# Optimization experiments

Hardware: AMD Instinct MI355X
Metric: run time of the kernel (lower is better)

The kernel has to match this reference:

```python
import jax, jax.numpy as jnp
import numpy as np

N_NODES = 100000
N_EDGES = 1600000
N_GRAPHS = 256
F_IN = 128
HID = 128


def gcn_conv(x, W, b, src, dst, n_nodes):
    """PyG GCNConv: h = D^{-1/2}(A+I)D^{-1/2} (x @ W) + b, self-loops added."""
    h = x @ W  # [N, H]
    ones = jnp.ones((src.shape[0],), dtype=x.dtype)
    deg = jax.ops.segment_sum(ones, dst, num_segments=n_nodes) + 1.0  # +1 self-loop
    dinv = jax.lax.rsqrt(deg)  # deg >= 1 always
    norm = dinv[src] * dinv[dst]  # [E]
    msgs = h[src] * norm[:, None]  # gather + scale, [E, H]
    agg = jax.ops.segment_sum(msgs, dst, num_segments=n_nodes)  # scatter-add
    agg = agg + h * (dinv * dinv)[:, None]  # self-loop contribution
    return agg + b


def setup_inputs() -> dict:
    key = jax.random.key(0)
    ks = jax.random.split(key, 8)
    x = jax.random.normal(ks[0], (N_NODES, F_IN), dtype=jnp.float32)
    edge_index = jax.random.randint(ks[1], (2, N_EDGES), 0, N_NODES, dtype=jnp.int64)
    batch = jnp.sort(jax.random.randint(ks[2], (N_NODES,), 0, N_GRAPHS, dtype=jnp.int64))
    s1 = 1.0 / np.sqrt(F_IN)
    s2 = 1.0 / np.sqrt(HID)
    w1 = jax.random.normal(ks[3], (F_IN, HID), dtype=jnp.float32) * s1
    b1 = jnp.zeros((HID,), dtype=jnp.float32)
    w2 = jax.random.normal(ks[4], (HID, HID), dtype=jnp.float32) * s2
    b2 = jnp.zeros((HID,), dtype=jnp.float32)
    w_out = jax.random.normal(ks[5], (HID, 1), dtype=jnp.float32) * s2
    b_out = jnp.zeros((1,), dtype=jnp.float32)
    return {"x": x, "edge_index": edge_index, "batch": batch,
            "w1": w1, "b1": b1, "w2": w2, "b2": b2,
            "w_out": w_out, "b_out": b_out}


def reference(x, edge_index, batch, w1, b1, w2, b2, w_out, b_out):
    src, dst = edge_index[0], edge_index[1]
    n = x.shape[0]
    h = jax.nn.relu(gcn_conv(x, w1, b1, src, dst, n))
    h = jax.nn.relu(gcn_conv(h, w2, b2, src, dst, n))
    # global mean pool over graphs
    sums = jax.ops.segment_sum(h, batch, num_segments=N_GRAPHS)  # [G, H]
    counts = jax.ops.segment_sum(jnp.ones((n,), dtype=h.dtype), batch, num_segments=N_GRAPHS)
    pooled = sums / jnp.maximum(counts, 1.0)[:, None]
    return pooled @ w_out + b_out  # [G, 1]
```

## Files before the change

### kernel.cpp

```cpp
#include <hip/hip_runtime.h>
#include <hip/hip_fp16.h>

#define N_NODES 100000
#define N_EDGES 1600000
#define N_GRAPHS 256
#define NB 1563
#define SBLOCKS 256
#define GB1 782

typedef _Float16 half8 __attribute__((ext_vector_type(8)));
typedef float f32x4 __attribute__((ext_vector_type(4)));

__device__ __forceinline__ unsigned pack2(float a, float b) {
    __half2 h = __floats2half2_rn(a, b);
    return *reinterpret_cast<unsigned*>(&h);
}

__global__ __launch_bounds__(256) void wprep_kernel(const float* __restrict__ W1,
                                                    const float* __restrict__ W2,
                                                    __half* __restrict__ Wt1,
                                                    __half* __restrict__ Wt2) {
    int b = blockIdx.x;
    const float* W = (b < 64) ? W1 : W2;
    __half* Wt = (b < 64) ? Wt1 : Wt2;
    int t = (b & 63) * 256 + threadIdx.x;
    int n = t >> 7, k = t & 127;
    Wt[t] = (__half)W[k * 128 + n];
}

__global__ __launch_bounds__(256) void gemmhist_kernel(const float* __restrict__ Xf,
                                                       const __half* __restrict__ Xh,
                                                       const __half* __restrict__ Wt,
                                                       const float* __restrict__ dinv,
                                                       __half* __restrict__ HT,
                                                       int xf16, int withDinv,
                                                       const int* __restrict__ dst,
                                                       int* __restrict__ cnt2d,
                                                       int histBlocks) {
    __shared__ __align__(16) char smem[69632];
    const int tid = threadIdx.x;
    int bid = blockIdx.x;
    bool isHist = false;
    int id = bid;
    if (histBlocks) {
        if (bid < 1024) {
            if ((bid & 3) == 0) { isHist = true; id = bid >> 2; }
            else id = (bid >> 2) * 3 + (bid & 3) - 1;
        } else {
            id = 768 + (bid - 1024);
        }
    }

    if (isHist) {
        int* lcnt = (int*)smem;
        for (int i = tid; i < NB; i += 256) lcnt[i] = 0;
        __syncthreads();
        const int per = (N_EDGES + SBLOCKS - 1) / SBLOCKS;
        int e0 = id * per, e1 = min(e0 + per, N_EDGES);
        for (int e = e0 + tid; e < e1; e += 256)
            atomicAdd(&lcnt[dst[e] >> 6], 1);
        __syncthreads();
        for (int i = tid; i < NB; i += 256)
            cnt2d[id * NB + i] = lcnt[i];
        return;
    }

    typedef __half (*TileT)[136];
    TileT Xl = (TileT)smem;
    TileT Wl = (TileT)(smem + 34816);
    const int row0 = id * 128;

#pragma unroll
    for (int i = 0; i < 8; ++i) {
        int idx = tid + i * 256;
        int n = idx >> 4, c0 = (idx & 15) * 8;
        *(uint4*)&Wl[n][c0] = *(const uint4*)&Wt[n * 128 + c0];
    }
    if (xf16) {
#pragma unroll
        for (int i = 0; i < 8; ++i) {
            int idx = tid + i * 256;
            int r = idx >> 4, c0 = (idx & 15) * 8;
            int rr = min(row0 + r, N_NODES - 1);
            *(uint4*)&Xl[r][c0] = *(const uint4*)&Xh[(size_t)rr * 128 + c0];
        }
    } else {
#pragma unroll
        for (int i = 0; i < 16; ++i) {
            int idx = tid + i * 256;
            int r = idx >> 5, c0 = (idx & 31) * 4;
            int rr = min(row0 + r, N_NODES - 1);
            float4 v = *(const float4*)&Xf[(size_t)rr * 128 + c0];
            uint2 o;
            o.x = pack2(v.x, v.y);
            o.y = pack2(v.z, v.w);
            *(uint2*)&Xl[r][c0] = o;
        }
    }
    __syncthreads();

    const int wv = tid >> 6;
    const int lane = tid & 63;
    const int lr = lane & 15;
    const int lg = lane >> 4;

    f32x4 acc[2][8];
#pragma unroll
    for (int mt = 0; mt < 2; ++mt)
#pragma unroll
        for (int nt = 0; nt < 8; ++nt) acc[mt][nt] = (f32x4){0.f, 0.f, 0.f, 0.f};

#pragma unroll
    for (int ks = 0; ks < 4; ++ks) {
        const int kb = ks * 32 + lg * 8;
        half8 a0 = *reinterpret_cast<const half8*>(&Xl[wv * 32 + lr][kb]);
        half8 a1 = *reinterpret_cast<const half8*>(&Xl[wv * 32 + 16 + lr][kb]);
        half8 b[8];
#pragma unroll
        for (int nt = 0; nt < 8; ++nt)
            b[nt] = *reinterpret_cast<const half8*>(&Wl[nt * 16 + lr][kb]);
#pragma unroll
        for (int nt = 0; nt < 8; ++nt) {
            acc[0][nt] = __builtin_amdgcn_mfma_f32_16x16x32_f16(a0, b[nt], acc[0][nt], 0, 0, 0);
            acc[1][nt] = __builtin_amdgcn_mfma_f32_16x16x32_f16(a1, b[nt], acc[1][nt], 0, 0, 0);
        }
    }

#pragma unroll
    for (int mt = 0; mt < 2; ++mt) {
#pragma unroll
        for (int i = 0; i < 4; ++i) {
            int rr = row0 + wv * 32 + mt * 16 + lg * 4 + i;
            if (rr < N_NODES) {
                float di = withDinv ? dinv[rr] : 1.0f;
#pragma unroll
                for (int nt = 0; nt < 8; ++nt)
                    HT[(size_t)rr * 128 + nt * 16 + lr] = (__half)(acc[mt][nt][i] * di);
            }
        }
    }
}

__global__ __launch_bounds__(256) void scan2d_kernel(int* __restrict__ cnt2d,
                                                     int* __restrict__ bucket_cnt) {
    __shared__ int ts[256];
    int i = blockIdx.x;
    int t = threadIdx.x;
    int v = cnt2d[t * NB + i];
    ts[t] = v;
    __syncthreads();
    for (int off = 1; off < 256; off <<= 1) {
        int y = (t >= off) ? ts[t - off] : 0;
        __syncthreads();
        ts[t] += y;
        __syncthreads();
    }
    cnt2d[t * NB + i] = ts[t] - v;
    if (t == 255) bucket_cnt[i] = ts[255];
}

#define BVPT 7
__global__ __launch_bounds__(256) void scatter_kernel(const int* __restrict__ src,
                                                      const int* __restrict__ dst,
                                                      const int* __restrict__ cnt2d,
                                                      const int* __restrict__ bucket_cnt,
                                                      int* __restrict__ bucket_off,
                                                      unsigned* __restrict__ pairbuf) {
    __shared__ int lcur[NB];
    __shared__ int tsum[256];
    const int tid = threadIdx.x;
    const int blk = blockIdx.x;

    int v[BVPT];
    int s = 0;
#pragma unroll
    for (int j = 0; j < BVPT; ++j) {
        int idx = tid * BVPT + j;
        v[j] = (idx < NB) ? bucket_cnt[idx] : 0;
        s += v[j];
    }
    tsum[tid] = s;
    __syncthreads();
    for (int off = 1; off < 256; off <<= 1) {
        int y = (tid >= off) ? tsum[tid - off] : 0;
        __syncthreads();
        tsum[tid] += y;
        __syncthreads();
    }
    int run = (tid > 0) ? tsum[tid - 1] : 0;
#pragma unroll
    for (int j = 0; j < BVPT; ++j) {
        int idx = tid * BVPT + j;
        if (idx < NB) {
            lcur[idx] = run + cnt2d[blk * NB + idx];
            if (blk == 0) bucket_off[idx] = run;
        }
        run += v[j];
    }
    if (blk == 0 && tid == 255) bucket_off[NB] = tsum[255];
    __syncthreads();

    const int per = (N_EDGES + SBLOCKS - 1) / SBLOCKS;
    int e0 = blk * per, e1 = min(e0 + per, N_EDGES);
    for (int e = e0 + tid; e < e1; e += 256) {
        int d = dst[e];
        int b = d >> 6;
        int p = atomicAdd(&lcur[b], 1);
        pairbuf[p] = ((unsigned)(d & 63) << 17) | (unsigned)src[e];
    }
}

__global__ __launch_bounds__(256) void localsort_kernel(const unsigned* __restrict__ pairbuf,
                                                        const int* __restrict__ bucket_off,
                                                        int* __restrict__ csr_src,
                                                        int* __restrict__ row_off,
                                                        float* __restrict__ dinv) {
    __shared__ int ldeg[64];
    __shared__ int lcur[64];
    int tid = threadIdx.x;
    int b = blockIdx.x;
    int base = bucket_off[b];
    int cnt = bucket_off[b + 1] - base;
    const unsigned* pb = pairbuf + base;
    int n0 = b << 6;

    if (tid < 64) ldeg[tid] = 0;
    __syncthreads();
    for (int i = tid; i < cnt; i += 256)
        atomicAdd(&ldeg[pb[i] >> 17], 1);
    __syncthreads();
    if (tid < 64) {
        int d = ldeg[tid];
        int x = d;
#pragma unroll
        for (int off = 1; off < 64; off <<= 1) {
            int y = __shfl_up(x, off);
            if (tid >= off) x += y;
        }
        int ex = x - d;
        lcur[tid] = ex;
        int n = n0 + tid;
        if (n < N_NODES) {
            row_off[n] = base + ex;
            dinv[n] = rsqrtf((float)d + 1.0f);
        }
    }
    __syncthreads();
    for (int i = tid; i < cnt; i += 256) {
        unsigned w = pb[i];
        int dl = w >> 17;
        int s = (int)(w & 0x1FFFFu);
        int p = atomicAdd(&lcur[dl], 1);
        csr_src[base + p] = s;
    }
}

__device__ __forceinline__ void add8(float* a, uint4 w) {
    float2 p0 = __half22float2(*reinterpret_cast<__half2*>(&w.x));
    float2 p1 = __half22float2(*reinterpret_cast<__half2*>(&w.y));
    float2 p2 = __half22float2(*reinterpret_cast<__half2*>(&w.z));
    float2 p3 = __half22float2(*reinterpret_cast<__half2*>(&w.w));
    a[0] += p0.x; a[1] += p0.y; a[2] += p1.x; a[3] += p1.y;
    a[4] += p2.x; a[5] += p2.y; a[6] += p3.x; a[7] += p3.y;
}
__device__ __forceinline__ void fma8(float* a, uint4 w, float s) {
    float2 p0 = __half22float2(*reinterpret_cast<__half2*>(&w.x));
    float2 p1 = __half22float2(*reinterpret_cast<__half2*>(&w.y));
    float2 p2 = __half22float2(*reinterpret_cast<__half2*>(&w.z));
    float2 p3 = __half22float2(*reinterpret_cast<__half2*>(&w.w));
    a[0] = fmaf(s, p0.x, a[0]); a[1] = fmaf(s, p0.y, a[1]);
    a[2] = fmaf(s, p1.x, a[2]); a[3] = fmaf(s, p1.y, a[3]);
    a[4] = fmaf(s, p2.x, a[4]); a[5] = fmaf(s, p2.y, a[5]);
    a[6] = fmaf(s, p3.x, a[6]); a[7] = fmaf(s, p3.y, a[7]);
}

__global__ __launch_bounds__(256) void gather1_kernel(const int* __restrict__ row_off,
                                                      const int* __restrict__ csr_src,
                                                      const __half* __restrict__ ht,
                                                      const float* __restrict__ dinv,
                                                      const float* __restrict__ bias,
                                                      __half* __restrict__ Y) {
    int t = blockIdx.x * 256 + threadIdx.x;
    int n = t >> 4;
    if (n >= N_NODES) return;
    int f = (t & 15) * 8;
    int e0 = row_off[n];
    int e1 = (n < N_NODES - 1) ? row_off[n + 1] : N_EDGES;
    const __half* htf = ht + f;
    float dn = dinv[n];

    float a0[8] = {0,0,0,0,0,0,0,0};
    float a1[8] = {0,0,0,0,0,0,0,0};
    float a2[8] = {0,0,0,0,0,0,0,0};
    float a3[8] = {0,0,0,0,0,0,0,0};
    fma8(a0, *(const uint4*)&htf[(size_t)n * 128], dn);

    int e = e0;
    for (; e + 4 <= e1; e += 4) {
        int s0 = csr_src[e], s1 = csr_src[e + 1];
        int s2 = csr_src[e + 2], s3 = csr_src[e + 3];
        uint4 w0 = *(const uint4*)&htf[(size_t)s0 * 128];
        uint4 w1 = *(const uint4*)&htf[(size_t)s1 * 128];
        uint4 w2 = *(const uint4*)&htf[(size_t)s2 * 128];
        uint4 w3 = *(const uint4*)&htf[(size_t)s3 * 128];
        fma8(a0, w0, dinv[s0]); fma8(a1, w1, dinv[s1]);
        fma8(a2, w2, dinv[s2]); fma8(a3, w3, dinv[s3]);
    }
    for (; e < e1; ++e) {
        int s = csr_src[e];
        fma8(a0, *(const uint4*)&htf[(size_t)s * 128], dinv[s]);
    }

    float4 bb0 = *(const float4*)&bias[f];
    float4 bb1 = *(const float4*)&bias[f + 4];
    float r0 = fmaxf((a0[0]+a1[0]+a2[0]+a3[0]) * dn + bb0.x, 0.0f);
    float r1 = fmaxf((a0[1]+a1[1]+a2[1]+a3[1]) * dn + bb0.y, 0.0f);
    float r2 = fmaxf((a0[2]+a1[2]+a2[2]+a3[2]) * dn + bb0.z, 0.0f);
    float r3 = fmaxf((a0[3]+a1[3]+a2[3]+a3[3]) * dn + bb0.w, 0.0f);
    float r4 = fmaxf((a0[4]+a1[4]+a2[4]+a3[4]) * dn + bb1.x, 0.0f);
    float r5 = fmaxf((a0[5]+a1[5]+a2[5]+a3[5]) * dn + bb1.y, 0.0f);
    float r6 = fmaxf((a0[6]+a1[6]+a2[6]+a3[6]) * dn + bb1.z, 0.0f);
    float r7 = fmaxf((a0[7]+a1[7]+a2[7]+a3[7]) * dn + bb1.w, 0.0f);
    uint4 o;
    o.x = pack2(r0, r1);
    o.y = pack2(r2, r3);
    o.z = pack2(r4, r5);
    o.w = pack2(r6, r7);
    *(uint4*)&Y[(size_t)n * 128 + f] = o;
}

__global__ __launch_bounds__(256) void gather2_kernel(const int* __restrict__ row_off,
                                                      const int* __restrict__ csr_src,
                                                      const __half* __restrict__ ht,
                                                      const float* __restrict__ dinv,
                                                      const float* __restrict__ bias,
                                                      __half* __restrict__ Y) {
    int t = blockIdx.x * 256 + threadIdx.x;
    int n = t >> 4;
    if (n >= N_NODES) return;
    int f = (t & 15) * 8;
    int e0 = row_off[n];
    int e1 = (n < N_NODES - 1) ? row_off[n + 1] : N_EDGES;
    const __half* htf = ht + f;
    float dn = dinv[n];

    float a0[8] = {0,0,0,0,0,0,0,0};
    float a1[8] = {0,0,0,0,0,0,0,0};
    float a2[8] = {0,0,0,0,0,0,0,0};
    float a3[8] = {0,0,0,0,0,0,0,0};
    add8(a0, *(const uint4*)&htf[(size_t)n * 128]);

    int e = e0;
    for (; e + 4 <= e1; e += 4) {
        int s0 = csr_src[e], s1 = csr_src[e + 1];
        int s2 = csr_src[e + 2], s3 = csr_src[e + 3];
        uint4 w0 = *(const uint4*)&htf[(size_t)s0 * 128];
        uint4 w1 = *(const uint4*)&htf[(size_t)s1 * 128];
        uint4 w2 = *(const uint4*)&htf[(size_t)s2 * 128];
        uint4 w3 = *(const uint4*)&htf[(size_t)s3 * 128];
        add8(a0, w0); add8(a1, w1); add8(a2, w2); add8(a3, w3);
    }
    for (; e < e1; ++e)
        add8(a0, *(const uint4*)&htf[(size_t)csr_src[e] * 128]);

    float4 bb0 = *(const float4*)&bias[f];
    float4 bb1 = *(const float4*)&bias[f + 4];
    float r0 = fmaxf((a0[0]+a1[0]+a2[0]+a3[0]) * dn + bb0.x, 0.0f);
    float r1 = fmaxf((a0[1]+a1[1]+a2[1]+a3[1]) * dn + bb0.y, 0.0f);
    float r2 = fmaxf((a0[2]+a1[2]+a2[2]+a3[2]) * dn + bb0.z, 0.0f);
    float r3 = fmaxf((a0[3]+a1[3]+a2[3]+a3[3]) * dn + bb0.w, 0.0f);
    float r4 = fmaxf((a0[4]+a1[4]+a2[4]+a3[4]) * dn + bb1.x, 0.0f);
    float r5 = fmaxf((a0[5]+a1[5]+a2[5]+a3[5]) * dn + bb1.y, 0.0f);
    float r6 = fmaxf((a0[6]+a1[6]+a2[6]+a3[6]) * dn + bb1.z, 0.0f);
    float r7 = fmaxf((a0[7]+a1[7]+a2[7]+a3[7]) * dn + bb1.w, 0.0f);
    uint4 o;
    o.x = pack2(r0, r1);
    o.y = pack2(r2, r3);
    o.z = pack2(r4, r5);
    o.w = pack2(r6, r7);
    *(uint4*)&Y[(size_t)n * 128 + f] = o;
}

__global__ __launch_bounds__(256) void poolout_kernel(const __half* __restrict__ Y,
                                                      const int* __restrict__ batch,
                                                      const float* __restrict__ w_out,
                                                      const float* __restrict__ b_out,
                                                      float* __restrict__ out) {
    __shared__ float red[8][128];
    __shared__ float pr[128];
    int g = blockIdx.x;
    int tid = threadIdx.x;
    int lo = 0, hi = N_NODES;
    while (lo < hi) { int m = (lo + hi) >> 1; if (batch[m] < g) lo = m + 1; else hi = m; }
    int lo2 = lo, hi2 = N_NODES;
    while (lo2 < hi2) { int m = (lo2 + hi2) >> 1; if (batch[m] < g + 1) lo2 = m + 1; else hi2 = m; }
    int cnt = lo2 - lo;

    int rslot = tid >> 5;
    int f = (tid & 31) * 4;
    float4 acc = make_float4(0, 0, 0, 0);
    for (int n = lo + rslot; n < lo2; n += 8) {
        uint2 w = *(const uint2*)&Y[(size_t)n * 128 + f];
        float2 p0 = __half22float2(*reinterpret_cast<__half2*>(&w.x));
        float2 p1 = __half22float2(*reinterpret_cast<__half2*>(&w.y));
        acc.x += p0.x; acc.y += p0.y; acc.z += p1.x; acc.w += p1.y;
    }
    *(float4*)&red[rslot][f] = acc;
    __syncthreads();
    if (tid < 128) {
        float s = 0.0f;
#pragma unroll
        for (int r = 0; r < 8; ++r) s += red[r][tid];
        pr[tid] = s * w_out[tid];
    }
    __syncthreads();
    for (int off = 64; off >= 1; off >>= 1) {
        if (tid < off) pr[tid] += pr[tid + off];
        __syncthreads();
    }
    if (tid == 0)
        out[g] = pr[0] / fmaxf((float)cnt, 1.0f) + b_out[0];
}

extern "C" void kernel_launch(void* const* d_in, const int* in_sizes, int n_in,
                              void* d_out, int out_size, void* d_ws, size_t ws_size,
                              hipStream_t stream) {
    const float* x     = (const float*)d_in[0];
    const int*   edge  = (const int*)d_in[1];
    const int*   batch = (const int*)d_in[2];
    const float* w1    = (const float*)d_in[3];
    const float* b1    = (const float*)d_in[4];
    const float* w2    = (const float*)d_in[5];
    const float* b2    = (const float*)d_in[6];
    const float* w_out = (const float*)d_in[7];
    const float* b_out = (const float*)d_in[8];
    float* out = (float*)d_out;

    char* ws = (char*)d_ws;
    size_t off = 0;
    auto alloc = [&](size_t bytes) {
        void* p = ws + off;
        off += (bytes + 511) & ~(size_t)511;
        return p;
    };
    const size_t FEAT_BYTES = (size_t)N_NODES * 128 * 4;
    __half*   ht16       = (__half*)alloc(FEAT_BYTES / 2);
    __half*   y16        = (__half*)alloc(FEAT_BYTES / 2);
    unsigned* pairbuf    = (unsigned*)y16;
    float*    dinv       = (float*)alloc(N_NODES * 4);
    int*      row_off    = (int*)alloc(N_NODES * 4);
    int*      csr_src    = (int*)alloc(N_EDGES * 4);
    int*      cnt2d      = (int*)alloc((size_t)SBLOCKS * NB * 4);
    int*      bucket_cnt = (int*)alloc((NB + 1) * 4);
    int*      bucket_off = (int*)alloc((NB + 1) * 4);
    __half*   wt1        = (__half*)alloc(128 * 128 * 2);
    __half*   wt2        = (__half*)alloc(128 * 128 * 2);

    const int* src = edge;
    const int* dst = edge + N_EDGES;

    wprep_kernel<<<128, 256, 0, stream>>>(w1, w2, wt1, wt2);

    gemmhist_kernel<<<1024 + (GB1 - 768), 256, 0, stream>>>(
        x, (const __half*)nullptr, wt1, (const float*)nullptr, ht16,
        0, 0, dst, cnt2d, 1);

    scan2d_kernel<<<NB, 256, 0, stream>>>(cnt2d, bucket_cnt);
    scatter_kernel<<<SBLOCKS, 256, 0, stream>>>(src, dst, cnt2d, bucket_cnt,
                                                bucket_off, pairbuf);
    localsort_kernel<<<NB, 256, 0, stream>>>(pairbuf, bucket_off, csr_src, row_off, dinv);

    gather1_kernel<<<(N_NODES * 16 + 255) / 256, 256, 0, stream>>>(
        row_off, csr_src, ht16, dinv, b1, y16);

    gemmhist_kernel<<<GB1, 256, 0, stream>>>(
        (const float*)nullptr, y16, wt2, dinv, ht16, 1, 1,
        (const int*)nullptr, (int*)nullptr, 0);
    gather2_kernel<<<(N_NODES * 16 + 255) / 256, 256, 0, stream>>>(
        row_off, csr_src, ht16, dinv, b2, y16);

    poolout_kernel<<<N_GRAPHS, 256, 0, stream>>>(y16, batch, w_out, b_out, out);
}
```

Before: 233.1 us.

## Fuse mean-pool and output projection into second gather via per-graph atomics

Instead of writing the second-layer activations to memory and re-reading them in a pooling kernel, the second gather kernel now dots each node's ReLU output with w_out, reduces across the 16 lanes, and atomically adds per-graph partial sums. It relies on the sorted batch vector to merge runs within a block before issuing atomics. A tiny finalize kernel divides by the node counts and adds the bias. This removes a full fp16 feature write and read plus one launch, at the cost of a __syncthreads, float atomics whose ordering is nondeterministic, and zeroing of the accumulator in the weight-prep kernel.

Result: no change. 234.4 us (+0.5%).

```diff
diff --git a/kernel.cpp b/kernel.cpp
--- a/kernel.cpp
+++ b/kernel.cpp
@@ -19,8 +19,10 @@
 __global__ __launch_bounds__(256) void wprep_kernel(const float* __restrict__ W1,
                                                     const float* __restrict__ W2,
                                                     __half* __restrict__ Wt1,
-                                                    __half* __restrict__ Wt2) {
+                                                    __half* __restrict__ Wt2,
+                                                    float* __restrict__ gacc) {
     int b = blockIdx.x;
+    if (b == 0) gacc[threadIdx.x] = 0.0f;
     const float* W = (b < 64) ? W1 : W2;
     __half* Wt = (b < 64) ? Wt1 : Wt2;
     int t = (b & 63) * 256 + threadIdx.x;
@@ -334,10 +336,13 @@
                                                       const __half* __restrict__ ht,
                                                       const float* __restrict__ dinv,
                                                       const float* __restrict__ bias,
-                                                      __half* __restrict__ Y) {
+                                                      const int* __restrict__ batch,
+                                                      const float* __restrict__ w_out,
+                                                      float* __restrict__ gacc) {
+    __shared__ float sdot[16];
+    __shared__ int   sg[16];
     int t = blockIdx.x * 256 + threadIdx.x;
     int n = t >> 4;
-    if (n >= N_NODES) return;
     int f = (t & 15) * 8;
     int e0 = row_off[n];
     int e1 = (n < N_NODES - 1) ? row_off[n + 1] : N_EDGES;
@@ -365,6 +370,8 @@
 
     float4 bb0 = *(const float4*)&bias[f];
     float4 bb1 = *(const float4*)&bias[f + 4];
+    float4 ww0 = *(const float4*)&w_out[f];
+    float4 ww1 = *(const float4*)&w_out[f + 4];
     float r0 = fmaxf((a0[0]+a1[0]+a2[0]+a3[0]) * dn + bb0.x, 0.0f);
     float r1 = fmaxf((a0[1]+a1[1]+a2[1]+a3[1]) * dn + bb0.y, 0.0f);
     float r2 = fmaxf((a0[2]+a1[2]+a2[2]+a3[2]) * dn + bb0.z, 0.0f);
@@ -373,53 +380,42 @@
     float r5 = fmaxf((a0[5]+a1[5]+a2[5]+a3[5]) * dn + bb1.y, 0.0f);
     float r6 = fmaxf((a0[6]+a1[6]+a2[6]+a3[6]) * dn + bb1.z, 0.0f);
     float r7 = fmaxf((a0[7]+a1[7]+a2[7]+a3[7]) * dn + bb1.w, 0.0f);
-    uint4 o;
-    o.x = pack2(r0, r1);
-    o.y = pack2(r2, r3);
-    o.z = pack2(r4, r5);
-    o.w = pack2(r6, r7);
-    *(uint4*)&Y[(size_t)n * 128 + f] = o;
-}
-
-__global__ __launch_bounds__(256) void poolout_kernel(const __half* __restrict__ Y,
-                                                      const int* __restrict__ batch,
-                                                      const float* __restrict__ w_out,
-                                                      const float* __restrict__ b_out,
-                                                      float* __restrict__ out) {
-    __shared__ float red[8][128];
-    __shared__ float pr[128];
-    int g = blockIdx.x;
+
+    float dot = r0*ww0.x + r1*ww0.y + r2*ww0.z + r3*ww0.w
+              + r4*ww1.x + r5*ww1.y + r6*ww1.z + r7*ww1.w;
+#pragma unroll
+    for (int off = 8; off >= 1; off >>= 1)
+        dot += __shfl_xor(dot, off);
+
     int tid = threadIdx.x;
+    if ((tid & 15) == 0) {
+        sdot[tid >> 4] = dot;
+        sg[tid >> 4] = batch[n];
+    }
+    __syncthreads();
+    if (tid == 0) {
+        float run = sdot[0];
+        int cg = sg[0];
+#pragma unroll
+        for (int i = 1; i < 16; ++i) {
+            if (sg[i] == cg) run += sdot[i];
+            else { atomicAdd(&gacc[cg], run); cg = sg[i]; run = sdot[i]; }
+        }
+        atomicAdd(&gacc[cg], run);
+    }
+}
+
+__global__ __launch_bounds__(256) void finalize_kernel(const float* __restrict__ gacc,
+                                                       const int* __restrict__ batch,
+                                                       const float* __restrict__ b_out,
+                                                       float* __restrict__ out) {
+    int g = threadIdx.x;
     int lo = 0, hi = N_NODES;
     while (lo < hi) { int m = (lo + hi) >> 1; if (batch[m] < g) lo = m + 1; else hi = m; }
     int lo2 = lo, hi2 = N_NODES;
     while (lo2 < hi2) { int m = (lo2 + hi2) >> 1; if (batch[m] < g + 1) lo2 = m + 1; else hi2 = m; }
     int cnt = lo2 - lo;
-
-    int rslot = tid >> 5;
-    int f = (tid & 31) * 4;
-    float4 acc = make_float4(0, 0, 0, 0);
-    for (int n = lo + rslot; n < lo2; n += 8) {
-        uint2 w = *(const uint2*)&Y[(size_t)n * 128 + f];
-        float2 p0 = __half22float2(*reinterpret_cast<__half2*>(&w.x));
-        float2 p1 = __half22float2(*reinterpret_cast<__half2*>(&w.y));
-        acc.x += p0.x; acc.y += p0.y; acc.z += p1.x; acc.w += p1.y;
-    }
-    *(float4*)&red[rslot][f] = acc;
-    __syncthreads();
-    if (tid < 128) {
-        float s = 0.0f;
-#pragma unroll
-        for (int r = 0; r < 8; ++r) s += red[r][tid];
-        pr[tid] = s * w_out[tid];
-    }
-    __syncthreads();
-    for (int off = 64; off >= 1; off >>= 1) {
-        if (tid < off) pr[tid] += pr[tid + off];
-        __syncthreads();
-    }
-    if (tid == 0)
-        out[g] = pr[0] / fmaxf((float)cnt, 1.0f) + b_out[0];
+    out[g] = gacc[g] / fmaxf((float)cnt, 1.0f) + b_out[0];
 }
 
 extern "C" void kernel_launch(void* const* d_in, const int* in_sizes, int n_in,
@@ -455,11 +451,12 @@
     int*      bucket_off = (int*)alloc((NB + 1) * 4);
     __half*   wt1        = (__half*)alloc(128 * 128 * 2);
     __half*   wt2        = (__half*)alloc(128 * 128 * 2);
+    float*    gacc       = (float*)alloc(N_GRAPHS * 4);
 
     const int* src = edge;
     const int* dst = edge + N_EDGES;
 
-    wprep_kernel<<<128, 256, 0, stream>>>(w1, w2, wt1, wt2);
+    wprep_kernel<<<128, 256, 0, stream>>>(w1, w2, wt1, wt2, gacc);
 
     gemmhist_kernel<<<1024 + (GB1 - 768), 256, 0, stream>>>(
         x, (const __half*)nullptr, wt1, (const float*)nullptr, ht16,
@@ -476,8 +473,8 @@
     gemmhist_kernel<<<GB1, 256, 0, stream>>>(
         (const float*)nullptr, y16, wt2, dinv, ht16, 1, 1,
         (const int*)nullptr, (int*)nullptr, 0);
-    gather2_kernel<<<(N_NODES * 16 + 255) / 256, 256, 0, stream>>>(
-        row_off, csr_src, ht16, dinv, b2, y16);
-
-    poolout_kernel<<<N_GRAPHS, 256, 0, stream>>>(y16, batch, w_out, b_out, out);
-}
+    gather2_kernel<<<(N_NODES * 16) / 256, 256, 0, stream>>>(
+        row_off, csr_src, ht16, dinv, b2, batch, w_out, gacc);
+
+    finalize_kernel<<<1, 256, 0, stream>>>(gacc, batch, b_out, out);
+}
```
